# Kernel tuning notes

Hardware: AMD Instinct MI355X
Metric: run time of the kernel (lower is better)

The kernel has to match this reference:

```python
import jax, jax.numpy as jnp
import numpy as np

N = 16384
IMRATIO = 0.0732
MARGIN = 1.0


def setup_inputs() -> dict:
    key = jax.random.key(0)
    k1, k2 = jax.random.split(key)
    preds = jax.random.normal(k1, (N,), dtype=jnp.float32)
    targets = (jax.random.uniform(k2, (N,)) < IMRATIO).astype(jnp.int32)
    return {"preds": preds, "targets": targets}


def reference(preds, targets):
    # positive = preds[targets==1]; negative = preds[targets==0]
    # loss = mean over P x N pairs of (1 - (p_i - n_j))**2 + margin * relu(1 - (p_i - n_j))
    # Expressed jit-compatibly as a mask-weighted full pairwise reduction (same math).
    pos_w = (targets == 1).astype(preds.dtype)  # [N]
    neg_w = (targets == 0).astype(preds.dtype)  # [N]
    one_minus_diff = 1.0 - (preds[:, None] - preds[None, :])  # [N, N]
    vals = one_minus_diff * one_minus_diff + MARGIN * jax.nn.relu(one_minus_diff)
    w = pos_w[:, None] * neg_w[None, :]  # [N, N] pair indicator
    num_pairs = pos_w.sum() * neg_w.sum()
    return (vals * w).sum() / num_pairs
```

## Files before the change

### kernel.cpp

```cpp
#include <hip/hip_runtime.h>


#define NSEG  64
#define MAXP  4096

__device__ __forceinline__ double wave_reduce_f64(double v) {
    #pragma unroll
    for (int off = 32; off > 0; off >>= 1) v += __shfl_xor(v, off, 64);
    return v;
}

__device__ __forceinline__ float wave_reduce_f32(float v) {
    #pragma unroll
    for (int off = 32; off > 0; off >>= 1) v += __shfl_xor(v, off, 64);
    return v;
}

__global__ __launch_bounds__(256)
void aucm_scan(const float* __restrict__ preds,
               const int* __restrict__ tgt,
               int n,
               double* __restrict__ momPart,
               int* __restrict__ cnt,
               float* __restrict__ posSeg) {
    __shared__ float sPos[256];
    __shared__ int sCnt;
    __shared__ double sRed[4][4];

    const int tid = threadIdx.x;
    const int b   = blockIdx.x;
    const int wave = tid >> 6;
    if (tid == 0) sCnt = 0;
    __syncthreads();

    const int i = b * 256 + tid;
    float a = 0.f, a2 = 0.f, nv = 0.f, n2 = 0.f;
    if (i < n) {
        const float p = preds[i];
        if (tgt[i] == 1) {
            const float av = 1.0f - p;
            a = av; a2 = av * av;
            const int idx = atomicAdd(&sCnt, 1);
            sPos[idx] = av;
        } else {
            nv = p; n2 = p * p;
        }
    }
    __syncthreads();
    const int c = sCnt;
    if (tid < c) posSeg[b * 256 + tid] = sPos[tid];

    const float rA  = wave_reduce_f32(a);
    const float rA2 = wave_reduce_f32(a2);
    const float rN  = wave_reduce_f32(nv);
    const float rN2 = wave_reduce_f32(n2);
    if ((tid & 63) == 0) {
        sRed[wave][0] = (double)rA;  sRed[wave][1] = (double)rA2;
        sRed[wave][2] = (double)rN;  sRed[wave][3] = (double)rN2;
    }
    __syncthreads();
    if (tid == 0) {
        double t0 = 0, t1 = 0, t2 = 0, t3 = 0;
        #pragma unroll
        for (int w = 0; w < 4; ++w) {
            t0 += sRed[w][0]; t1 += sRed[w][1];
            t2 += sRed[w][2]; t3 += sRed[w][3];
        }
        momPart[b * 4 + 0] = t0; momPart[b * 4 + 1] = t1;
        momPart[b * 4 + 2] = t2; momPart[b * 4 + 3] = t3;
        cnt[b] = c;
    }
}

__global__ __launch_bounds__(256)
void aucm_relu(const float* __restrict__ preds,
               const int* __restrict__ tgt,
               int n,
               const int* __restrict__ cnt,
               const float* __restrict__ posSeg,
               double* __restrict__ reluPart) {
    __shared__ int pref[NSEG + 1];
    __shared__ float sA[MAXP];
    __shared__ double sRed[4];

    const int tid   = threadIdx.x;
    const int jb    = blockIdx.x & 63;
    const int slice = blockIdx.x >> 6;

    if (tid == 0) {
        int run = 0;
        for (int s = 0; s < NSEG; ++s) { pref[s] = run; run += cnt[s]; }
        pref[NSEG] = run;
    }
    __syncthreads();

    const int total = pref[NSEG];
    const int per   = (total + 3) >> 2;
    const int lo    = slice * per;
    const int hi    = min(total, lo + per);
    const int cntS  = max(0, hi - lo);

    for (int s = tid; s < cntS; s += 256) {
        const int g = lo + s;
        int l = 0, h = NSEG;
        while (h - l > 1) { const int m = (l + h) >> 1; if (pref[m] <= g) l = m; else h = m; }
        sA[s] = posSeg[l * 256 + (g - pref[l])];
    }
    __syncthreads();

    const int j = jb * 256 + tid;
    float acc = 0.f;
    if (j < n && tgt[j] == 0) {
        const float pj = preds[j];
        int k = 0;
        for (; k + 8 <= cntS; k += 8) {
            #pragma unroll
            for (int u = 0; u < 8; ++u)
                acc += fmaxf(sA[k + u] + pj, 0.f);
        }
        for (; k < cntS; ++k) acc += fmaxf(sA[k] + pj, 0.f);
    }

    double r = wave_reduce_f64((double)acc);
    if ((tid & 63) == 0) sRed[tid >> 6] = r;
    __syncthreads();
    if (tid == 0)
        reluPart[blockIdx.x] = sRed[0] + sRed[1] + sRed[2] + sRed[3];
}

__global__ __launch_bounds__(256)
void aucm_fin(const double* __restrict__ momPart,
              const int* __restrict__ cnt,
              const double* __restrict__ reluPart,
              int nRelu, int n,
              float* __restrict__ out, float margin) {
    __shared__ double sRed[4][6];
    const int tid = threadIdx.x;
    const int wave = tid >> 6;

    double mA = 0, mA2 = 0, mN = 0, mN2 = 0, r = 0, pc = 0;
    for (int i = tid; i < NSEG; i += 256) {
        mA  += momPart[i * 4 + 0]; mA2 += momPart[i * 4 + 1];
        mN  += momPart[i * 4 + 2]; mN2 += momPart[i * 4 + 3];
        pc  += (double)cnt[i];
    }
    for (int i = tid; i < nRelu; i += 256) r += reluPart[i];

    mA = wave_reduce_f64(mA);  mA2 = wave_reduce_f64(mA2);
    mN = wave_reduce_f64(mN);  mN2 = wave_reduce_f64(mN2);
    r  = wave_reduce_f64(r);   pc  = wave_reduce_f64(pc);
    if ((tid & 63) == 0) {
        sRed[wave][0] = mA; sRed[wave][1] = mA2; sRed[wave][2] = mN;
        sRed[wave][3] = mN2; sRed[wave][4] = r;  sRed[wave][5] = pc;
    }
    __syncthreads();
    if (tid == 0) {
        double tA = 0, tA2 = 0, tN = 0, tN2 = 0, tR = 0, tP = 0;
        #pragma unroll
        for (int w = 0; w < 4; ++w) {
            tA += sRed[w][0]; tA2 += sRed[w][1]; tN += sRed[w][2];
            tN2 += sRed[w][3]; tR += sRed[w][4]; tP += sRed[w][5];
        }
        const double P  = tP;
        const double Nn = (double)n - tP;
        const double sq = Nn * tA2 + 2.0 * tA * tN + P * tN2;
        out[0] = (float)((sq + (double)margin * tR) / (P * Nn));
    }
}

extern "C" void kernel_launch(void* const* d_in, const int* in_sizes, int n_in,
                              void* d_out, int out_size, void* d_ws, size_t ws_size,
                              hipStream_t stream) {
    const float* preds = (const float*)d_in[0];
    const int*   tgt   = (const int*)d_in[1];
    float* out = (float*)d_out;
    const int n = in_sizes[0];

    char* ws = (char*)d_ws;
    double* momPart  = (double*)(ws + 0);
    int*    cnt      = (int*)(ws + 2048);
    double* reluPart = (double*)(ws + 2304);
    float*  posSeg   = (float*)(ws + 4352);

    aucm_scan<<<NSEG, 256, 0, stream>>>(preds, tgt, n, momPart, cnt, posSeg);
    aucm_relu<<<NSEG * 4, 256, 0, stream>>>(preds, tgt, n, cnt, posSeg, reluPart);
    aucm_fin<<<1, 256, 0, stream>>>(momPart, cnt, reluPart, NSEG * 4, n, out,
                                    1.0f );
}
```

Before: 66.66 us.

## Fuse scan, relu and finalize kernels into one cooperative kernel with grid syncs

Merges the three kernel launches into a single cooperative launch of 256 blocks that separates the phases with grid-wide barriers. This removes two kernel launch gaps and inter-kernel dependencies. It also replaces the serial prefix sum with a wave shuffle scan and reads the shared positive array as float4. The trade-off is the cost of each grid sync, the requirement that all blocks be co-resident, and block 0 doing the final reduction alone.

```diff
diff --git a/kernel.cpp b/kernel.cpp
--- a/kernel.cpp
+++ b/kernel.cpp
@@ -1,4 +1,7 @@
 #include <hip/hip_runtime.h>
+#include <hip/hip_cooperative_groups.h>
+
+namespace cg = cooperative_groups;
 
 
 #define NSEG  64
@@ -17,80 +20,82 @@
 }
 
 __global__ __launch_bounds__(256)
-void aucm_scan(const float* __restrict__ preds,
-               const int* __restrict__ tgt,
-               int n,
-               double* __restrict__ momPart,
-               int* __restrict__ cnt,
-               float* __restrict__ posSeg) {
-    __shared__ float sPos[256];
+void aucm_fused(const float* __restrict__ preds,
+                const int* __restrict__ tgt,
+                int n,
+                double* __restrict__ momPart,
+                int* __restrict__ cnt,
+                float* __restrict__ posSeg,
+                double* __restrict__ reluPart,
+                float* __restrict__ out,
+                float margin)
+{
+    __shared__ __align__(16) float sA[MAXP];
+    __shared__ int pref[NSEG + 1];
+    __shared__ double sRed[4][6];
     __shared__ int sCnt;
-    __shared__ double sRed[4][4];
 
-    const int tid = threadIdx.x;
-    const int b   = blockIdx.x;
+    const int tid  = threadIdx.x;
+    const int b    = blockIdx.x;
     const int wave = tid >> 6;
-    if (tid == 0) sCnt = 0;
-    __syncthreads();
 
-    const int i = b * 256 + tid;
-    float a = 0.f, a2 = 0.f, nv = 0.f, n2 = 0.f;
-    if (i < n) {
-        const float p = preds[i];
-        if (tgt[i] == 1) {
-            const float av = 1.0f - p;
-            a = av; a2 = av * av;
-            const int idx = atomicAdd(&sCnt, 1);
-            sPos[idx] = av;
-        } else {
-            nv = p; n2 = p * p;
+    if (b < NSEG) {
+        if (tid == 0) sCnt = 0;
+        __syncthreads();
+
+        const int i = b * 256 + tid;
+        float a = 0.f, a2 = 0.f, nv = 0.f, n2 = 0.f;
+        if (i < n) {
+            const float p = preds[i];
+            if (tgt[i] == 1) {
+                const float av = 1.0f - p;
+                a = av; a2 = av * av;
+                const int idx = atomicAdd(&sCnt, 1);
+                sA[idx] = av;
+            } else {
+                nv = p; n2 = p * p;
+            }
+        }
+        __syncthreads();
+        const int c = sCnt;
+        if (tid < c) posSeg[b * 256 + tid] = sA[tid];
+
+        const float rA  = wave_reduce_f32(a);
+        const float rA2 = wave_reduce_f32(a2);
+        const float rN  = wave_reduce_f32(nv);
+        const float rN2 = wave_reduce_f32(n2);
+        if ((tid & 63) == 0) {
+            sRed[wave][0] = (double)rA;  sRed[wave][1] = (double)rA2;
+            sRed[wave][2] = (double)rN;  sRed[wave][3] = (double)rN2;
+        }
+        __syncthreads();
+        if (tid == 0) {
+            double t0 = 0, t1 = 0, t2 = 0, t3 = 0;
+            #pragma unroll
+            for (int w = 0; w < 4; ++w) {
+                t0 += sRed[w][0]; t1 += sRed[w][1];
+                t2 += sRed[w][2]; t3 += sRed[w][3];
+            }
+            momPart[b * 4 + 0] = t0; momPart[b * 4 + 1] = t1;
+            momPart[b * 4 + 2] = t2; momPart[b * 4 + 3] = t3;
+            cnt[b] = c;
         }
     }
-    __syncthreads();
-    const int c = sCnt;
-    if (tid < c) posSeg[b * 256 + tid] = sPos[tid];
 
-    const float rA  = wave_reduce_f32(a);
-    const float rA2 = wave_reduce_f32(a2);
-    const float rN  = wave_reduce_f32(nv);
-    const float rN2 = wave_reduce_f32(n2);
-    if ((tid & 63) == 0) {
-        sRed[wave][0] = (double)rA;  sRed[wave][1] = (double)rA2;
-        sRed[wave][2] = (double)rN;  sRed[wave][3] = (double)rN2;
-    }
-    __syncthreads();
-    if (tid == 0) {
-        double t0 = 0, t1 = 0, t2 = 0, t3 = 0;
+    cg::this_grid().sync();
+
+    const int jb    = b & 63;
+    const int slice = b >> 6;
+
+    if (tid < 64) {
+        int s = cnt[tid];
         #pragma unroll
-        for (int w = 0; w < 4; ++w) {
-            t0 += sRed[w][0]; t1 += sRed[w][1];
-            t2 += sRed[w][2]; t3 += sRed[w][3];
+        for (int d = 1; d < 64; d <<= 1) {
+            const int up = __shfl_up(s, d, 64);
+            if (tid >= d) s += up;
         }
-        momPart[b * 4 + 0] = t0; momPart[b * 4 + 1] = t1;
-        momPart[b * 4 + 2] = t2; momPart[b * 4 + 3] = t3;
-        cnt[b] = c;
-    }
-}
-
-__global__ __launch_bounds__(256)
-void aucm_relu(const float* __restrict__ preds,
-               const int* __restrict__ tgt,
-               int n,
-               const int* __restrict__ cnt,
-               const float* __restrict__ posSeg,
-               double* __restrict__ reluPart) {
-    __shared__ int pref[NSEG + 1];
-    __shared__ float sA[MAXP];
-    __shared__ double sRed[4];
-
-    const int tid   = threadIdx.x;
-    const int jb    = blockIdx.x & 63;
-    const int slice = blockIdx.x >> 6;
-
-    if (tid == 0) {
-        int run = 0;
-        for (int s = 0; s < NSEG; ++s) { pref[s] = run; run += cnt[s]; }
-        pref[NSEG] = run;
+        pref[tid + 1] = s;
+        if (tid == 0) pref[0] = 0;
     }
     __syncthreads();
 
@@ -114,57 +119,57 @@
         const float pj = preds[j];
         int k = 0;
         for (; k + 8 <= cntS; k += 8) {
-            #pragma unroll
-            for (int u = 0; u < 8; ++u)
-                acc += fmaxf(sA[k + u] + pj, 0.f);
+            const float4 v0 = *reinterpret_cast<const float4*>(&sA[k]);
+            const float4 v1 = *reinterpret_cast<const float4*>(&sA[k + 4]);
+            acc += fmaxf(v0.x + pj, 0.f);
+            acc += fmaxf(v0.y + pj, 0.f);
+            acc += fmaxf(v0.z + pj, 0.f);
+            acc += fmaxf(v0.w + pj, 0.f);
+            acc += fmaxf(v1.x + pj, 0.f);
+            acc += fmaxf(v1.y + pj, 0.f);
+            acc += fmaxf(v1.z + pj, 0.f);
+            acc += fmaxf(v1.w + pj, 0.f);
         }
         for (; k < cntS; ++k) acc += fmaxf(sA[k] + pj, 0.f);
     }
 
     double r = wave_reduce_f64((double)acc);
-    if ((tid & 63) == 0) sRed[tid >> 6] = r;
+    if ((tid & 63) == 0) sRed[wave][0] = r;
     __syncthreads();
     if (tid == 0)
-        reluPart[blockIdx.x] = sRed[0] + sRed[1] + sRed[2] + sRed[3];
-}
+        reluPart[b] = sRed[0][0] + sRed[1][0] + sRed[2][0] + sRed[3][0];
 
-__global__ __launch_bounds__(256)
-void aucm_fin(const double* __restrict__ momPart,
-              const int* __restrict__ cnt,
-              const double* __restrict__ reluPart,
-              int nRelu, int n,
-              float* __restrict__ out, float margin) {
-    __shared__ double sRed[4][6];
-    const int tid = threadIdx.x;
-    const int wave = tid >> 6;
+    cg::this_grid().sync();
 
-    double mA = 0, mA2 = 0, mN = 0, mN2 = 0, r = 0, pc = 0;
-    for (int i = tid; i < NSEG; i += 256) {
-        mA  += momPart[i * 4 + 0]; mA2 += momPart[i * 4 + 1];
-        mN  += momPart[i * 4 + 2]; mN2 += momPart[i * 4 + 3];
-        pc  += (double)cnt[i];
-    }
-    for (int i = tid; i < nRelu; i += 256) r += reluPart[i];
+    if (b == 0) {
+        double mA = 0, mA2 = 0, mN = 0, mN2 = 0, rr = 0, pc = 0;
+        for (int i = tid; i < NSEG; i += 256) {
+            mA  += momPart[i * 4 + 0]; mA2 += momPart[i * 4 + 1];
+            mN  += momPart[i * 4 + 2]; mN2 += momPart[i * 4 + 3];
+            pc  += (double)cnt[i];
+        }
+        for (int i = tid; i < NSEG * 4; i += 256) rr += reluPart[i];
 
-    mA = wave_reduce_f64(mA);  mA2 = wave_reduce_f64(mA2);
-    mN = wave_reduce_f64(mN);  mN2 = wave_reduce_f64(mN2);
-    r  = wave_reduce_f64(r);   pc  = wave_reduce_f64(pc);
-    if ((tid & 63) == 0) {
-        sRed[wave][0] = mA; sRed[wave][1] = mA2; sRed[wave][2] = mN;
-        sRed[wave][3] = mN2; sRed[wave][4] = r;  sRed[wave][5] = pc;
-    }
-    __syncthreads();
-    if (tid == 0) {
-        double tA = 0, tA2 = 0, tN = 0, tN2 = 0, tR = 0, tP = 0;
-        #pragma unroll
-        for (int w = 0; w < 4; ++w) {
-            tA += sRed[w][0]; tA2 += sRed[w][1]; tN += sRed[w][2];
-            tN2 += sRed[w][3]; tR += sRed[w][4]; tP += sRed[w][5];
+        mA = wave_reduce_f64(mA);  mA2 = wave_reduce_f64(mA2);
+        mN = wave_reduce_f64(mN);  mN2 = wave_reduce_f64(mN2);
+        rr = wave_reduce_f64(rr);  pc  = wave_reduce_f64(pc);
+        if ((tid & 63) == 0) {
+            sRed[wave][0] = mA; sRed[wave][1] = mA2; sRed[wave][2] = mN;
+            sRed[wave][3] = mN2; sRed[wave][4] = rr; sRed[wave][5] = pc;
         }
-        const double P  = tP;
-        const double Nn = (double)n - tP;
-        const double sq = Nn * tA2 + 2.0 * tA * tN + P * tN2;
-        out[0] = (float)((sq + (double)margin * tR) / (P * Nn));
+        __syncthreads();
+        if (tid == 0) {
+            double tA = 0, tA2 = 0, tN = 0, tN2 = 0, tR = 0, tP = 0;
+            #pragma unroll
+            for (int w = 0; w < 4; ++w) {
+                tA += sRed[w][0]; tA2 += sRed[w][1]; tN += sRed[w][2];
+                tN2 += sRed[w][3]; tR += sRed[w][4]; tP += sRed[w][5];
+            }
+            const double P  = tP;
+            const double Nn = (double)n - tP;
+            const double sq = Nn * tA2 + 2.0 * tA * tN + P * tN2;
+            out[0] = (float)((sq + (double)margin * tR) / (P * Nn));
+        }
     }
 }
 
@@ -174,16 +179,19 @@
     const float* preds = (const float*)d_in[0];
     const int*   tgt   = (const int*)d_in[1];
     float* out = (float*)d_out;
-    const int n = in_sizes[0];
+    int n = in_sizes[0];
 
     char* ws = (char*)d_ws;
     double* momPart  = (double*)(ws + 0);
     int*    cnt      = (int*)(ws + 2048);
     double* reluPart = (double*)(ws + 2304);
     float*  posSeg   = (float*)(ws + 4352);
+    float margin = 1.0f;
 
-    aucm_scan<<<NSEG, 256, 0, stream>>>(preds, tgt, n, momPart, cnt, posSeg);
-    aucm_relu<<<NSEG * 4, 256, 0, stream>>>(preds, tgt, n, cnt, posSeg, reluPart);
-    aucm_fin<<<1, 256, 0, stream>>>(momPart, cnt, reluPart, NSEG * 4, n, out,
-                                    1.0f );
+    void* args[] = { (void*)&preds, (void*)&tgt, (void*)&n, (void*)&momPart,
+                     (void*)&cnt, (void*)&posSeg, (void*)&reluPart,
+                     (void*)&out, (void*)&margin };
+
+    hipLaunchCooperativeKernel((const void*)aucm_fused, dim3(NSEG * 4), dim3(256),
+                               args, 0, stream);
 }
```

After: 124.7 us. +87.1%, slower.

## Fuse final reduction into relu kernel via last-block atomic counter

Applied to the files above, without the earlier changes.

Removes the separate single-block finalize kernel: each relu block publishes its partial with a release store and bumps a global counter, and the last block to arrive reduces all partials and writes the output. The counter is reset in the scan kernel. It also replaces the serial prefix sum with a wave shuffle scan, vectorizes the shared-memory reads with float4 using two accumulators, and accumulates in double per 64-element chunk. This saves a kernel launch and a dependency bubble, at the cost of atomics and memory-ordering complexity.

```diff
diff --git a/kernel.cpp b/kernel.cpp
--- a/kernel.cpp
+++ b/kernel.cpp
@@ -22,7 +22,8 @@
                int n,
                double* __restrict__ momPart,
                int* __restrict__ cnt,
-               float* __restrict__ posSeg) {
+               float* __restrict__ posSeg,
+               int* __restrict__ counter) {
     __shared__ float sPos[256];
     __shared__ int sCnt;
     __shared__ double sRed[4][4];
@@ -69,6 +70,9 @@
         momPart[b * 4 + 0] = t0; momPart[b * 4 + 1] = t1;
         momPart[b * 4 + 2] = t2; momPart[b * 4 + 3] = t3;
         cnt[b] = c;
+        if (b == 0)
+            __hip_atomic_store(counter, 0, __ATOMIC_RELEASE,
+                               __HIP_MEMORY_SCOPE_AGENT);
     }
 }
 
@@ -78,19 +82,31 @@
                int n,
                const int* __restrict__ cnt,
                const float* __restrict__ posSeg,
-               double* __restrict__ reluPart) {
+               const double* __restrict__ momPart,
+               double* __restrict__ reluPart,
+               int* __restrict__ counter,
+               float* __restrict__ out, float margin) {
     __shared__ int pref[NSEG + 1];
-    __shared__ float sA[MAXP];
-    __shared__ double sRed[4];
+    __shared__ __align__(16) float sA[MAXP];
+    __shared__ double sRed[4][6];
+    __shared__ int sLast;
 
     const int tid   = threadIdx.x;
-    const int jb    = blockIdx.x & 63;
-    const int slice = blockIdx.x >> 6;
-
-    if (tid == 0) {
-        int run = 0;
-        for (int s = 0; s < NSEG; ++s) { pref[s] = run; run += cnt[s]; }
-        pref[NSEG] = run;
+    const int lane  = tid & 63;
+    const int wave  = tid >> 6;
+    const int b     = blockIdx.x;
+    const int jb    = b & 63;
+    const int slice = b >> 6;
+
+    if (tid < 64) {
+        int s = cnt[tid];
+        #pragma unroll
+        for (int d = 1; d < 64; d <<= 1) {
+            const int t = __shfl_up(s, d, 64);
+            if (lane >= d) s += t;
+        }
+        pref[tid + 1] = s;
+        if (tid == 0) pref[0] = 0;
     }
     __syncthreads();
 
@@ -108,63 +124,75 @@
     }
     __syncthreads();
 
-    const int j = jb * 256 + tid;
-    float acc = 0.f;
+    const int j = (jb << 8) + tid;
+    double accd = 0.0;
     if (j < n && tgt[j] == 0) {
         const float pj = preds[j];
         int k = 0;
-        for (; k + 8 <= cntS; k += 8) {
+        while (k < cntS) {
+            const int end = min(cntS, k + 64);
+            float a0 = 0.f, a1 = 0.f;
+            for (; k + 8 <= end; k += 8) {
+                const float4 v0 = *reinterpret_cast<const float4*>(&sA[k]);
+                const float4 v1 = *reinterpret_cast<const float4*>(&sA[k + 4]);
+                a0 += fmaxf(v0.x + pj, 0.f);
+                a1 += fmaxf(v0.y + pj, 0.f);
+                a0 += fmaxf(v0.z + pj, 0.f);
+                a1 += fmaxf(v0.w + pj, 0.f);
+                a0 += fmaxf(v1.x + pj, 0.f);
+                a1 += fmaxf(v1.y + pj, 0.f);
+                a0 += fmaxf(v1.z + pj, 0.f);
+                a1 += fmaxf(v1.w + pj, 0.f);
+            }
+            float at = a0 + a1;
+            for (; k < end; ++k) at += fmaxf(sA[k] + pj, 0.f);
+            accd += (double)at;
+        }
+    }
+
+    double r = wave_reduce_f64(accd);
+    if (lane == 0) sRed[wave][0] = r;
+    __syncthreads();
+    if (tid == 0) {
+        const double part = sRed[0][0] + sRed[1][0] + sRed[2][0] + sRed[3][0];
+        __hip_atomic_store(&reluPart[b], part, __ATOMIC_RELEASE,
+                           __HIP_MEMORY_SCOPE_AGENT);
+        const int old = __hip_atomic_fetch_add(counter, 1, __ATOMIC_ACQ_REL,
+                                               __HIP_MEMORY_SCOPE_AGENT);
+        sLast = (old == NSEG * 4 - 1);
+    }
+    __syncthreads();
+
+    if (sLast) {
+        double mA = 0, mA2 = 0, mN = 0, mN2 = 0, rr = 0;
+        for (int i = tid; i < NSEG; i += 256) {
+            mA  += momPart[i * 4 + 0]; mA2 += momPart[i * 4 + 1];
+            mN  += momPart[i * 4 + 2]; mN2 += momPart[i * 4 + 3];
+        }
+        for (int i = tid; i < NSEG * 4; i += 256)
+            rr += __hip_atomic_load(&reluPart[i], __ATOMIC_RELAXED,
+                                    __HIP_MEMORY_SCOPE_AGENT);
+
+        mA = wave_reduce_f64(mA);  mA2 = wave_reduce_f64(mA2);
+        mN = wave_reduce_f64(mN);  mN2 = wave_reduce_f64(mN2);
+        rr = wave_reduce_f64(rr);
+        if (lane == 0) {
+            sRed[wave][1] = mA; sRed[wave][2] = mA2;
+            sRed[wave][3] = mN; sRed[wave][4] = mN2; sRed[wave][5] = rr;
+        }
+        __syncthreads();
+        if (tid == 0) {
+            double tA = 0, tA2 = 0, tN = 0, tN2 = 0, tR = 0;
             #pragma unroll
-            for (int u = 0; u < 8; ++u)
-                acc += fmaxf(sA[k + u] + pj, 0.f);
-        }
-        for (; k < cntS; ++k) acc += fmaxf(sA[k] + pj, 0.f);
-    }
-
-    double r = wave_reduce_f64((double)acc);
-    if ((tid & 63) == 0) sRed[tid >> 6] = r;
-    __syncthreads();
-    if (tid == 0)
-        reluPart[blockIdx.x] = sRed[0] + sRed[1] + sRed[2] + sRed[3];
-}
-
-__global__ __launch_bounds__(256)
-void aucm_fin(const double* __restrict__ momPart,
-              const int* __restrict__ cnt,
-              const double* __restrict__ reluPart,
-              int nRelu, int n,
-              float* __restrict__ out, float margin) {
-    __shared__ double sRed[4][6];
-    const int tid = threadIdx.x;
-    const int wave = tid >> 6;
-
-    double mA = 0, mA2 = 0, mN = 0, mN2 = 0, r = 0, pc = 0;
-    for (int i = tid; i < NSEG; i += 256) {
-        mA  += momPart[i * 4 + 0]; mA2 += momPart[i * 4 + 1];
-        mN  += momPart[i * 4 + 2]; mN2 += momPart[i * 4 + 3];
-        pc  += (double)cnt[i];
-    }
-    for (int i = tid; i < nRelu; i += 256) r += reluPart[i];
-
-    mA = wave_reduce_f64(mA);  mA2 = wave_reduce_f64(mA2);
-    mN = wave_reduce_f64(mN);  mN2 = wave_reduce_f64(mN2);
-    r  = wave_reduce_f64(r);   pc  = wave_reduce_f64(pc);
-    if ((tid & 63) == 0) {
-        sRed[wave][0] = mA; sRed[wave][1] = mA2; sRed[wave][2] = mN;
-        sRed[wave][3] = mN2; sRed[wave][4] = r;  sRed[wave][5] = pc;
-    }
-    __syncthreads();
-    if (tid == 0) {
-        double tA = 0, tA2 = 0, tN = 0, tN2 = 0, tR = 0, tP = 0;
-        #pragma unroll
-        for (int w = 0; w < 4; ++w) {
-            tA += sRed[w][0]; tA2 += sRed[w][1]; tN += sRed[w][2];
-            tN2 += sRed[w][3]; tR += sRed[w][4]; tP += sRed[w][5];
-        }
-        const double P  = tP;
-        const double Nn = (double)n - tP;
-        const double sq = Nn * tA2 + 2.0 * tA * tN + P * tN2;
-        out[0] = (float)((sq + (double)margin * tR) / (P * Nn));
+            for (int w = 0; w < 4; ++w) {
+                tA += sRed[w][1]; tA2 += sRed[w][2]; tN += sRed[w][3];
+                tN2 += sRed[w][4]; tR += sRed[w][5];
+            }
+            const double P  = (double)total;
+            const double Nn = (double)n - P;
+            const double sq = Nn * tA2 + 2.0 * tA * tN + P * tN2;
+            out[0] = (float)((sq + (double)margin * tR) / (P * Nn));
+        }
     }
 }
 
@@ -180,10 +208,12 @@
     double* momPart  = (double*)(ws + 0);
     int*    cnt      = (int*)(ws + 2048);
     double* reluPart = (double*)(ws + 2304);
-    float*  posSeg   = (float*)(ws + 4352);
-
-    aucm_scan<<<NSEG, 256, 0, stream>>>(preds, tgt, n, momPart, cnt, posSeg);
-    aucm_relu<<<NSEG * 4, 256, 0, stream>>>(preds, tgt, n, cnt, posSeg, reluPart);
-    aucm_fin<<<1, 256, 0, stream>>>(momPart, cnt, reluPart, NSEG * 4, n, out,
-                                    1.0f );
-}
+    int*    counter  = (int*)(ws + 4352);
+    float*  posSeg   = (float*)(ws + 4608);
+
+    aucm_scan<<<NSEG, 256, 0, stream>>>(preds, tgt, n, momPart, cnt, posSeg,
+                                        counter);
+    aucm_relu<<<NSEG * 4, 256, 0, stream>>>(preds, tgt, n, cnt, posSeg,
+                                            momPart, reluPart, counter, out,
+                                            1.0f );
+}
```

Result: slower. 72.14 us (+8.2%).
